# Kernel tuning notes

Measured on AMD Instinct MI355X. Metric: run time of the kernel, lower is better.

The kernel has to match this reference:

```python
import jax, jax.numpy as jnp
import numpy as np

EPS = 1e-5  # torch LayerNorm default
N_BLOCKS = 8
N_NODES = 4096
BATCH = 4096


def setup_inputs() -> dict:
    key = jax.random.key(0)
    ks = jax.random.split(key, 4)
    scale = 1.0 / np.sqrt(N_NODES)  # keep activations sane through 8 GEMMs
    x = jax.random.normal(ks[0], (BATCH, N_NODES), dtype=jnp.float32)
    W = jax.random.normal(ks[1], (N_BLOCKS, N_NODES, N_NODES), dtype=jnp.float32) * scale
    b = jax.random.normal(ks[2], (N_BLOCKS, N_NODES), dtype=jnp.float32) * 0.01
    slope = jax.random.uniform(ks[3], (N_BLOCKS, N_NODES), dtype=jnp.float32)
    ln_g = jnp.ones((N_BLOCKS, N_NODES), dtype=jnp.float32)
    ln_b = jnp.zeros((N_BLOCKS, N_NODES), dtype=jnp.float32)
    return {"x": x, "ln_g": ln_g, "ln_b": ln_b, "W": W, "b": b, "slope": slope}


def _block(x, g, bt, Wi, bi, si):
    # LayerNorm over last dim (biased variance, eps inside sqrt) -> Linear -> per-feature LeakyReLU
    mu = jnp.mean(x, axis=-1, keepdims=True)
    var = jnp.mean(jnp.square(x - mu), axis=-1, keepdims=True)
    ln = (x - mu) * jax.lax.rsqrt(var + EPS) * g + bt
    y = jnp.einsum('bn,mn->bm', ln, Wi) + bi  # torch Linear: x @ W.T + b
    return jnp.where(y < 0, y * si, y)


def reference(x, ln_g, ln_b, W, b, slope):
    for i in range(N_BLOCKS):
        x = _block(x, ln_g[i], ln_b[i], W[i], b[i], slope[i])
    return x
```

## Files before the change

### kernel.cpp

```cpp
#include <hip/hip_runtime.h>
#include <hip/hip_bf16.h>

#define NNODES 4096
#define NBATCH 4096
#define NBLK 8
#define LN_EPS 1e-5f

typedef __attribute__((ext_vector_type(8))) short short8;
typedef __attribute__((ext_vector_type(4))) float f32x4;
typedef __attribute__((ext_vector_type(4))) unsigned short u16x4;
typedef unsigned short u16;

__device__ __forceinline__ u16 bf16_rn(float f) {
  unsigned int u = __builtin_bit_cast(unsigned int, f);
  u += 0x7fffu + ((u >> 16) & 1u);
  return (u16)(u >> 16);
}

__device__ __forceinline__ float bf16_to_f(u16 h) {
  unsigned int u = ((unsigned int)h) << 16;
  return __builtin_bit_cast(float, u);
}

__device__ __forceinline__ void load_lds16(const void* g, void* l) {
  __builtin_amdgcn_global_load_lds((const __attribute__((address_space(1))) void*)g,
                                   (__attribute__((address_space(3))) void*)l,
                                   16, 0, 0);
}

__device__ __forceinline__ void stage_sub(const u16* g, u16* l) {
  load_lds16(g, l);
  load_lds16(g + (size_t)128 * NNODES, l + 4096);
}

template <bool LNF32>
__global__ __launch_bounds__(256) void prep_kernel(const float* __restrict__ W,
                                                   u16* __restrict__ Wb,
                                                   const void* __restrict__ xin,
                                                   const float* __restrict__ g,
                                                   const float* __restrict__ bt,
                                                   u16* __restrict__ lnout) {
  __shared__ float sh[8];
  int t = threadIdx.x;
  if (blockIdx.x < 16384) {
    int idx = blockIdx.x * 256 + t;
    float4 v = ((const float4*)W)[idx];
    u16x4 o;
    o[0] = bf16_rn(v.x); o[1] = bf16_rn(v.y); o[2] = bf16_rn(v.z); o[3] = bf16_rn(v.w);
    ((u16x4*)Wb)[idx] = o;
    return;
  }
  int row = blockIdx.x - 16384;
  float f[16];
  float s = 0.f, ss = 0.f;
  if constexpr (LNF32) {
    const float4* xr = (const float4*)((const float*)xin + (size_t)row * NNODES);
#pragma unroll
    for (int q = 0; q < 4; ++q) {
      float4 v = xr[q * 256 + t];
      f[q * 4 + 0] = v.x; f[q * 4 + 1] = v.y; f[q * 4 + 2] = v.z; f[q * 4 + 3] = v.w;
      s  += v.x + v.y + v.z + v.w;
      ss += v.x * v.x + v.y * v.y + v.z * v.z + v.w * v.w;
    }
  } else {
    const u16* xr = (const u16*)xin + (size_t)row * NNODES;
#pragma unroll
    for (int q = 0; q < 2; ++q) {
      short8 v = *(const short8*)(xr + q * 2048 + t * 8);
#pragma unroll
      for (int j = 0; j < 8; ++j) {
        float fv = bf16_to_f((u16)v[j]);
        f[q * 8 + j] = fv;
        s += fv; ss += fv * fv;
      }
    }
  }
#pragma unroll
  for (int off = 32; off >= 1; off >>= 1) {
    s  += __shfl_xor(s, off, 64);
    ss += __shfl_xor(ss, off, 64);
  }
  int wid = t >> 6, lane = t & 63;
  if (lane == 0) { sh[wid] = s; sh[wid + 4] = ss; }
  __syncthreads();
  s  = sh[0] + sh[1] + sh[2] + sh[3];
  ss = sh[4] + sh[5] + sh[6] + sh[7];
  float mu  = s * (1.f / NNODES);
  float var = ss * (1.f / NNODES) - mu * mu;
  float rs  = rsqrtf(var + LN_EPS);
  const float* gp = g;
  const float* bp = bt;
  if constexpr (LNF32) {
    u16x4* o = (u16x4*)(lnout + (size_t)row * NNODES);
    const float4* gv = (const float4*)gp;
    const float4* bv = (const float4*)bp;
#pragma unroll
    for (int q = 0; q < 4; ++q) {
      int i = q * 256 + t;
      float4 gg = gv[i], bb = bv[i];
      u16x4 ov;
      ov[0] = bf16_rn((f[q * 4 + 0] - mu) * rs * gg.x + bb.x);
      ov[1] = bf16_rn((f[q * 4 + 1] - mu) * rs * gg.y + bb.y);
      ov[2] = bf16_rn((f[q * 4 + 2] - mu) * rs * gg.z + bb.z);
      ov[3] = bf16_rn((f[q * 4 + 3] - mu) * rs * gg.w + bb.w);
      o[i] = ov;
    }
  } else {
#pragma unroll
    for (int q = 0; q < 2; ++q) {
      int base = q * 2048 + t * 8;
      float4 g0 = ((const float4*)gp)[base / 4], g1 = ((const float4*)gp)[base / 4 + 1];
      float4 b0 = ((const float4*)bp)[base / 4], b1 = ((const float4*)bp)[base / 4 + 1];
      short8 sv;
      sv[0] = (short)bf16_rn((f[q * 8 + 0] - mu) * rs * g0.x + b0.x);
      sv[1] = (short)bf16_rn((f[q * 8 + 1] - mu) * rs * g0.y + b0.y);
      sv[2] = (short)bf16_rn((f[q * 8 + 2] - mu) * rs * g0.z + b0.z);
      sv[3] = (short)bf16_rn((f[q * 8 + 3] - mu) * rs * g0.w + b0.w);
      sv[4] = (short)bf16_rn((f[q * 8 + 4] - mu) * rs * g1.x + b1.x);
      sv[5] = (short)bf16_rn((f[q * 8 + 5] - mu) * rs * g1.y + b1.y);
      sv[6] = (short)bf16_rn((f[q * 8 + 6] - mu) * rs * g1.z + b1.z);
      sv[7] = (short)bf16_rn((f[q * 8 + 7] - mu) * rs * g1.w + b1.w);
      *(short8*)(lnout + (size_t)row * NNODES + base) = sv;
    }
  }
}

template <bool OUTF32>
__global__ __launch_bounds__(512, 2) void gemm256_kernel(const u16* __restrict__ A,
                                                         const u16* __restrict__ B,
                                                         const float* __restrict__ bias,
                                                         const float* __restrict__ slope,
                                                         void* __restrict__ Cv) {
  constexpr int Kdim = NNODES;
  constexpr int NSUB = Kdim / 32;
  __shared__ u16 Alds[4][8192];
  __shared__ u16 Blds[4][8192];

  const int tid  = threadIdx.x;
  const int lane = tid & 63;
  const int wid  = tid >> 6;
  const int wr   = wid >> 2;
  const int wc   = wid & 3;

  int bid = blockIdx.x;
  int swz = (bid & 7) * 32 + (bid >> 3);
  const int brow = (swz >> 4) * 256;
  const int bcol = (swz & 15) * 256;

  const int srow = tid >> 2;
  const int scsw = (tid & 3) ^ ((srow >> 1) & 3);
  const u16* Ag = A + (size_t)(brow + srow) * Kdim + scsw * 8;
  const u16* Bg = B + (size_t)(bcol + srow) * Kdim + scsw * 8;

  const int r16 = lane & 15, kq = lane >> 4;
  const int ck  = kq ^ ((r16 >> 1) & 3);
  const int aoff = (wr * 128 + r16) * 32 + ck * 8;
  const int boff = (wc * 64 + r16) * 32 + ck * 8;

  f32x4 acc[8][4] = {};

#pragma unroll
  for (int s = 0; s < 3; ++s) {
    stage_sub(Ag + s * 32, &Alds[s][0] + tid * 8);
    stage_sub(Bg + s * 32, &Blds[s][0] + tid * 8);
  }
  asm volatile("s_waitcnt vmcnt(8)" ::: "memory");
  __builtin_amdgcn_s_barrier();

  for (int s = 0; s < NSUB; ++s) {
    const int sl = s & 3;
    const u16* abase = &Alds[sl][0] + aoff;
    const u16* bbase = &Blds[sl][0] + boff;
    short8 a03[4], a47[4], bfr[4];

#pragma unroll
    for (int n = 0; n < 4; ++n) bfr[n] = *(const short8*)(bbase + n * 512);
#pragma unroll
    for (int m = 0; m < 4; ++m) a03[m] = *(const short8*)(abase + m * 512);
    __builtin_amdgcn_sched_barrier(0);
#pragma unroll
    for (int m = 0; m < 4; ++m) a47[m] = *(const short8*)(abase + (m + 4) * 512);

    if (s + 3 < NSUB) {
      stage_sub(Ag + (s + 3) * 32, &Alds[(s + 3) & 3][0] + tid * 8);
      stage_sub(Bg + (s + 3) * 32, &Blds[(s + 3) & 3][0] + tid * 8);
    }
    if (s <= NSUB - 4)      asm volatile("s_waitcnt vmcnt(8)" ::: "memory");
    else if (s == NSUB - 3) asm volatile("s_waitcnt vmcnt(4)" ::: "memory");
    else if (s == NSUB - 2) asm volatile("s_waitcnt vmcnt(0)" ::: "memory");

    asm volatile("s_waitcnt lgkmcnt(4)" ::: "memory");
    __builtin_amdgcn_sched_barrier(0);
    __builtin_amdgcn_s_setprio(1);
#pragma unroll
    for (int m = 0; m < 4; ++m)
#pragma unroll
      for (int n = 0; n < 4; ++n)
        acc[m][n] = __builtin_amdgcn_mfma_f32_16x16x32_bf16(a03[m], bfr[n], acc[m][n], 0, 0, 0);
    __builtin_amdgcn_s_setprio(0);

    asm volatile("s_waitcnt lgkmcnt(0)" ::: "memory");
    __builtin_amdgcn_sched_barrier(0);
    __builtin_amdgcn_s_setprio(1);
#pragma unroll
    for (int m = 0; m < 4; ++m)
#pragma unroll
      for (int n = 0; n < 4; ++n)
        acc[m + 4][n] = __builtin_amdgcn_mfma_f32_16x16x32_bf16(a47[m], bfr[n], acc[m + 4][n], 0, 0, 0);
    __builtin_amdgcn_s_setprio(0);
    __builtin_amdgcn_s_barrier();
  }

  const int crow0 = brow + wr * 128 + (lane >> 4) * 4;
  const int ccol0 = bcol + wc * 64 + r16;
#pragma unroll
  for (int n = 0; n < 4; ++n) {
    int col = ccol0 + n * 16;
    float bv = bias[col], sv = slope[col];
#pragma unroll
    for (int m = 0; m < 8; ++m) {
      int row0 = crow0 + m * 16;
#pragma unroll
      for (int r = 0; r < 4; ++r) {
        float vv = acc[m][n][r] + bv;
        vv = vv < 0.f ? vv * sv : vv;
        if constexpr (OUTF32) {
          ((float*)Cv)[(size_t)(row0 + r) * NNODES + col] = vv;
        } else {
          ((u16*)Cv)[(size_t)(row0 + r) * NNODES + col] = bf16_rn(vv);
        }
      }
    }
  }
}

extern "C" void kernel_launch(void* const* d_in, const int* in_sizes, int n_in,
                              void* d_out, int out_size, void* d_ws, size_t ws_size,
                              hipStream_t stream) {
  const float* x     = (const float*)d_in[0];
  const float* ln_g  = (const float*)d_in[1];
  const float* ln_b  = (const float*)d_in[2];
  const float* W     = (const float*)d_in[3];
  const float* b     = (const float*)d_in[4];
  const float* slope = (const float*)d_in[5];
  float* out = (float*)d_out;

  char* ws = (char*)d_ws;
  u16* Wbuf  = (u16*)ws;
  u16* lnbuf = (u16*)(ws + (size_t)32 * 1024 * 1024);
  u16* ybuf  = (u16*)(ws + (size_t)64 * 1024 * 1024);

  const size_t WN = (size_t)NNODES * NNODES;
  const dim3 pgrid(16384 + NBATCH);

  for (int i = 0; i < NBLK; ++i) {
    if (i == 0)
      prep_kernel<true><<<pgrid, dim3(256), 0, stream>>>(W, Wbuf, (const void*)x,
                                                         ln_g, ln_b, lnbuf);
    else
      prep_kernel<false><<<pgrid, dim3(256), 0, stream>>>(W + WN * i, Wbuf, (const void*)ybuf,
                                                          ln_g + (size_t)i * NNODES,
                                                          ln_b + (size_t)i * NNODES, lnbuf);
    if (i == NBLK - 1)
      gemm256_kernel<true><<<dim3(256), dim3(512), 0, stream>>>(lnbuf, Wbuf,
                                                                b + (size_t)i * NNODES,
                                                                slope + (size_t)i * NNODES, (void*)out);
    else
      gemm256_kernel<false><<<dim3(256), dim3(512), 0, stream>>>(lnbuf, Wbuf,
                                                                 b + (size_t)i * NNODES,
                                                                 slope + (size_t)i * NNODES, (void*)ybuf);
  }
}
```

Baseline: 1.182 ms.

## Restructure GEMM mainloop into 64-wide K tiles with 8-phase ping-pong schedule

Replaces the 4-stage ring of 32-wide K slices with double-buffered 64-wide K tiles, split into quadrant phases that interleave global-to-LDS staging of A and B halves with MFMA work on the current tile. The LDS swizzle is changed to an 8-way XOR to suit the 128-byte rows. The intent is to issue fewer, larger loads per barrier and to hide memory latency behind compute in a finer-grained way. In exchange there are more barriers per K step, and the hand-tuned vmcnt accounting is fragile and could cause stalls or races if a count is wrong.

```diff
diff --git a/kernel.cpp b/kernel.cpp
--- a/kernel.cpp
+++ b/kernel.cpp
@@ -26,11 +26,6 @@
   __builtin_amdgcn_global_load_lds((const __attribute__((address_space(1))) void*)g,
                                    (__attribute__((address_space(3))) void*)l,
                                    16, 0, 0);
-}
-
-__device__ __forceinline__ void stage_sub(const u16* g, u16* l) {
-  load_lds16(g, l);
-  load_lds16(g + (size_t)128 * NNODES, l + 4096);
 }
 
 template <bool LNF32>
@@ -88,12 +83,10 @@
   float mu  = s * (1.f / NNODES);
   float var = ss * (1.f / NNODES) - mu * mu;
   float rs  = rsqrtf(var + LN_EPS);
-  const float* gp = g;
-  const float* bp = bt;
   if constexpr (LNF32) {
     u16x4* o = (u16x4*)(lnout + (size_t)row * NNODES);
-    const float4* gv = (const float4*)gp;
-    const float4* bv = (const float4*)bp;
+    const float4* gv = (const float4*)g;
+    const float4* bv = (const float4*)bt;
 #pragma unroll
     for (int q = 0; q < 4; ++q) {
       int i = q * 256 + t;
@@ -109,8 +102,8 @@
 #pragma unroll
     for (int q = 0; q < 2; ++q) {
       int base = q * 2048 + t * 8;
-      float4 g0 = ((const float4*)gp)[base / 4], g1 = ((const float4*)gp)[base / 4 + 1];
-      float4 b0 = ((const float4*)bp)[base / 4], b1 = ((const float4*)bp)[base / 4 + 1];
+      float4 g0 = ((const float4*)g)[base / 4], g1 = ((const float4*)g)[base / 4 + 1];
+      float4 b0 = ((const float4*)bt)[base / 4], b1 = ((const float4*)bt)[base / 4 + 1];
       short8 sv;
       sv[0] = (short)bf16_rn((f[q * 8 + 0] - mu) * rs * g0.x + b0.x);
       sv[1] = (short)bf16_rn((f[q * 8 + 1] - mu) * rs * g0.y + b0.y);
@@ -125,6 +118,58 @@
   }
 }
 
+
+#define VMC(N) asm volatile("s_waitcnt vmcnt(" #N ")" ::: "memory")
+
+#define STAGE_A(T, H)                                                          \
+  { load_lds16(Asrc0 + (size_t)((H) * 128) * Kdim + (T) * 64,                  \
+               ldsA + ((T) & 1) * 16384 + (H) * 8192 + tid * 8);               \
+    load_lds16(Asrc0 + (size_t)((H) * 128 + 64) * Kdim + (T) * 64,             \
+               ldsA + ((T) & 1) * 16384 + (H) * 8192 + 4096 + tid * 8); }
+
+#define STAGE_B(T, H)                                                          \
+  { load_lds16(Bsrc0 + (size_t)((H) * 128) * Kdim + (T) * 64,                  \
+               ldsB + ((T) & 1) * 16384 + (H) * 8192 + tid * 8);               \
+    load_lds16(Bsrc0 + (size_t)((H) * 128 + 64) * Kdim + (T) * 64,             \
+               ldsB + ((T) & 1) * 16384 + (H) * 8192 + 4096 + tid * 8); }
+
+#define PH(KT, MH, NH, STAGE_STMT, VM_STMT)                                    \
+  {                                                                            \
+    const u16* Ab = ldsA + ((KT) & 1) * 16384 + aBase + (MH) * 4096;           \
+    const u16* Bb = ldsB + ((KT) & 1) * 16384 + bBase + (NH) * 2048;           \
+    if ((NH) == 0) {                                                           \
+      _Pragma("unroll") for (int mi = 0; mi < 4; ++mi) {                       \
+        afr[mi][0] = *(const short8*)(Ab + mi * 1024 + gk0);                   \
+        afr[mi][1] = *(const short8*)(Ab + mi * 1024 + gk1);                   \
+      }                                                                        \
+    }                                                                          \
+    if ((MH) == 0) {                                                           \
+      _Pragma("unroll") for (int ni = 0; ni < 2; ++ni) {                       \
+        bfr[NH][ni][0] = *(const short8*)(Bb + ni * 1024 + gk0);               \
+        bfr[NH][ni][1] = *(const short8*)(Bb + ni * 1024 + gk1);               \
+      }                                                                        \
+    }                                                                          \
+    STAGE_STMT;                                                                \
+    if ((NH) == 0 && (MH) == 0)                                                \
+      asm volatile("s_waitcnt lgkmcnt(8)" ::: "memory");                       \
+    VM_STMT;                                                                   \
+    __builtin_amdgcn_s_barrier();                                              \
+    asm volatile("s_waitcnt lgkmcnt(0)" ::: "memory");                         \
+    __builtin_amdgcn_sched_barrier(0);                                         \
+    __builtin_amdgcn_s_setprio(1);                                             \
+    _Pragma("unroll") for (int mi = 0; mi < 4; ++mi)                           \
+      _Pragma("unroll") for (int ni = 0; ni < 2; ++ni) {                       \
+        acc[(MH) * 4 + mi][(NH) * 2 + ni] =                                    \
+          __builtin_amdgcn_mfma_f32_16x16x32_bf16(afr[mi][0], bfr[NH][ni][0],  \
+            acc[(MH) * 4 + mi][(NH) * 2 + ni], 0, 0, 0);                       \
+        acc[(MH) * 4 + mi][(NH) * 2 + ni] =                                    \
+          __builtin_amdgcn_mfma_f32_16x16x32_bf16(afr[mi][1], bfr[NH][ni][1],  \
+            acc[(MH) * 4 + mi][(NH) * 2 + ni], 0, 0, 0);                       \
+      }                                                                        \
+    __builtin_amdgcn_s_setprio(0);                                             \
+    __builtin_amdgcn_s_barrier();                                              \
+  }
+
 template <bool OUTF32>
 __global__ __launch_bounds__(512, 2) void gemm256_kernel(const u16* __restrict__ A,
                                                          const u16* __restrict__ B,
@@ -132,9 +177,9 @@
                                                          const float* __restrict__ slope,
                                                          void* __restrict__ Cv) {
   constexpr int Kdim = NNODES;
-  constexpr int NSUB = Kdim / 32;
-  __shared__ u16 Alds[4][8192];
-  __shared__ u16 Blds[4][8192];
+  __shared__ u16 lds[65536];
+  u16* ldsA = lds;
+  u16* ldsB = lds + 32768;
 
   const int tid  = threadIdx.x;
   const int lane = tid & 63;
@@ -147,69 +192,43 @@
   const int brow = (swz >> 4) * 256;
   const int bcol = (swz & 15) * 256;
 
-  const int srow = tid >> 2;
-  const int scsw = (tid & 3) ^ ((srow >> 1) & 3);
-  const u16* Ag = A + (size_t)(brow + srow) * Kdim + scsw * 8;
-  const u16* Bg = B + (size_t)(bcol + srow) * Kdim + scsw * 8;
+  const int srow = tid >> 3;
+  const int sg   = ((tid & 7) ^ (srow & 7)) * 8;
+  const u16* Asrc0 = A + (size_t)(brow + srow) * Kdim + sg;
+  const u16* Bsrc0 = B + (size_t)(bcol + srow) * Kdim + sg;
 
   const int r16 = lane & 15, kq = lane >> 4;
-  const int ck  = kq ^ ((r16 >> 1) & 3);
-  const int aoff = (wr * 128 + r16) * 32 + ck * 8;
-  const int boff = (wc * 64 + r16) * 32 + ck * 8;
+  const int g0  = kq ^ (r16 & 7);
+  const int gk0 = g0 * 8, gk1 = (g0 ^ 4) * 8;
+  const int aBase = wr * 8192 + r16 * 64;
+  const int bBase = (wc >> 1) * 8192 + ((wc & 1) * 64 + r16) * 64;
 
   f32x4 acc[8][4] = {};
-
-#pragma unroll
-  for (int s = 0; s < 3; ++s) {
-    stage_sub(Ag + s * 32, &Alds[s][0] + tid * 8);
-    stage_sub(Bg + s * 32, &Blds[s][0] + tid * 8);
-  }
-  asm volatile("s_waitcnt vmcnt(8)" ::: "memory");
+  short8 afr[4][2], bfr[2][2][2];
+
+  STAGE_B(0, 0) STAGE_B(0, 1) STAGE_A(0, 0) STAGE_A(0, 1) STAGE_B(1, 0) STAGE_B(1, 1)
+  VMC(4);
   __builtin_amdgcn_s_barrier();
 
-  for (int s = 0; s < NSUB; ++s) {
-    const int sl = s & 3;
-    const u16* abase = &Alds[sl][0] + aoff;
-    const u16* bbase = &Blds[sl][0] + boff;
-    short8 a03[4], a47[4], bfr[4];
-
-#pragma unroll
-    for (int n = 0; n < 4; ++n) bfr[n] = *(const short8*)(bbase + n * 512);
-#pragma unroll
-    for (int m = 0; m < 4; ++m) a03[m] = *(const short8*)(abase + m * 512);
-    __builtin_amdgcn_sched_barrier(0);
-#pragma unroll
-    for (int m = 0; m < 4; ++m) a47[m] = *(const short8*)(abase + (m + 4) * 512);
-
-    if (s + 3 < NSUB) {
-      stage_sub(Ag + (s + 3) * 32, &Alds[(s + 3) & 3][0] + tid * 8);
-      stage_sub(Bg + (s + 3) * 32, &Blds[(s + 3) & 3][0] + tid * 8);
-    }
-    if (s <= NSUB - 4)      asm volatile("s_waitcnt vmcnt(8)" ::: "memory");
-    else if (s == NSUB - 3) asm volatile("s_waitcnt vmcnt(4)" ::: "memory");
-    else if (s == NSUB - 2) asm volatile("s_waitcnt vmcnt(0)" ::: "memory");
-
-    asm volatile("s_waitcnt lgkmcnt(4)" ::: "memory");
-    __builtin_amdgcn_sched_barrier(0);
-    __builtin_amdgcn_s_setprio(1);
-#pragma unroll
-    for (int m = 0; m < 4; ++m)
-#pragma unroll
-      for (int n = 0; n < 4; ++n)
-        acc[m][n] = __builtin_amdgcn_mfma_f32_16x16x32_bf16(a03[m], bfr[n], acc[m][n], 0, 0, 0);
-    __builtin_amdgcn_s_setprio(0);
-
-    asm volatile("s_waitcnt lgkmcnt(0)" ::: "memory");
-    __builtin_amdgcn_sched_barrier(0);
-    __builtin_amdgcn_s_setprio(1);
-#pragma unroll
-    for (int m = 0; m < 4; ++m)
-#pragma unroll
-      for (int n = 0; n < 4; ++n)
-        acc[m + 4][n] = __builtin_amdgcn_mfma_f32_16x16x32_bf16(a47[m], bfr[n], acc[m + 4][n], 0, 0, 0);
-    __builtin_amdgcn_s_setprio(0);
-    __builtin_amdgcn_s_barrier();
-  }
+  for (int t = 0; t < 31; ++t) {
+    const int T = 2 * t;
+    PH(T,     0, 0, STAGE_A(T + 1, 0), ;)
+    PH(T,     0, 1, STAGE_A(T + 1, 1), ;)
+    PH(T,     1, 0, STAGE_B(T + 2, 0), ;)
+    PH(T,     1, 1, STAGE_B(T + 2, 1), VMC(4))
+    PH(T + 1, 0, 0, STAGE_A(T + 2, 0), ;)
+    PH(T + 1, 0, 1, STAGE_A(T + 2, 1), ;)
+    PH(T + 1, 1, 0, STAGE_B(T + 3, 0), ;)
+    PH(T + 1, 1, 1, STAGE_B(T + 3, 1), VMC(4))
+  }
+  PH(62, 0, 0, STAGE_A(63, 0), ;)
+  PH(62, 0, 1, STAGE_A(63, 1), ;)
+  PH(62, 1, 0, ;, ;)
+  PH(62, 1, 1, ;, VMC(0))
+  PH(63, 0, 0, ;, ;)
+  PH(63, 0, 1, ;, ;)
+  PH(63, 1, 0, ;, ;)
+  PH(63, 1, 1, ;, ;)
 
   const int crow0 = brow + wr * 128 + (lane >> 4) * 4;
   const int ccol0 = bcol + wc * 64 + r16;
```

After: 1.119 ms. -5.3%, faster.
